# Optimization experiments

Measured on AMD Instinct MI355X. Metric: run time of the kernel, lower is better.

## Reference

```python
import jax, jax.numpy as jnp
import numpy as np

HEADS = 8

def setup_inputs() -> dict:
    key = jax.random.key(0)
    ks = jax.random.split(key, 6)
    N, C, L = 8, 512, 2048
    s = 0.02
    return {
        'x':  jax.random.normal(ks[0], (N, C, L), dtype=jnp.float32),
        'Wq': jax.random.normal(ks[1], (C, C), dtype=jnp.float32) * s,
        'Wk': jax.random.normal(ks[2], (C, C), dtype=jnp.float32) * s,
        'Wv': jax.random.normal(ks[3], (C, C), dtype=jnp.float32) * s,
        'Wo': jax.random.normal(ks[4], (C, C), dtype=jnp.float32) * s,
        'bo': jnp.zeros((C,), dtype=jnp.float32),
    }

def reference(x, Wq, Wk, Wv, Wo, bo):
    N, C, L = x.shape
    h = HEADS
    d = C // h
    scale = C ** (-0.5)  # note: scales by full channels, as in the original

    def proj(W):
        # Conv1d(k=1, bias=False) == per-position linear: [N,C,L] -> [N,L,h,d]
        y = jnp.einsum('oc,ncl->nlo', W, x)
        return y.reshape(N, L, h, d)

    q, k, v = proj(Wq), proj(Wk), proj(Wv)

    qk = jnp.einsum('nqhd,nkhd->nhqk', q, k)  # [N,h,L,L]
    causal_mask = jnp.tril(jnp.ones((L, L), dtype=bool))
    qk = jnp.where(causal_mask, qk, -jnp.inf)
    attn = jax.nn.softmax(qk * scale, axis=-1)

    out = jnp.einsum('nhqk,nkhd->nqhd', attn, v)  # [N,L,h,d]
    out = out.reshape(N, L, C).transpose(0, 2, 1)  # n (h d) l
    return jnp.einsum('oc,ncl->nol', Wo, out) + bo[None, :, None]
```

## Files before the change

### kernel.cpp

```cpp
#include <hip/hip_runtime.h>
#include <math.h>

typedef __bf16 bf16;
typedef __attribute__((ext_vector_type(8))) __bf16 bf16x8;
typedef __attribute__((ext_vector_type(4))) float f32x4;
typedef unsigned short u16;
typedef unsigned int u32;

constexpr int Nn = 8, Cc = 512, Ll = 2048, Hh = 8, Dd = 64;
constexpr float kScale = 0.044194173824159216f;
constexpr float kQexp2 = kScale * 1.44269504088896341f;
constexpr size_t NCL = (size_t)Nn * Cc * Ll;
constexpr size_t WSZ = (size_t)Cc * Cc;

static __device__ __forceinline__ u16 bfbits(bf16 v) {
    union { bf16 b; u16 u; } x; x.b = v; return x.u;
}
static __device__ __forceinline__ u32 fbits(float f) {
    union { float f; u32 u; } x; x.f = f; return x.u;
}
static __device__ __forceinline__ float fexp2(float x) {
#if __has_builtin(__builtin_amdgcn_exp2f)
    return __builtin_amdgcn_exp2f(x);
#else
    return exp2f(x);
#endif
}

#define MFMA(a, b, c) __builtin_amdgcn_mfma_f32_16x16x32_bf16((a), (b), (c), 0, 0, 0)

static __device__ __forceinline__ void async16(const bf16* g, bf16* l) {
    __builtin_amdgcn_global_load_lds(
        (const __attribute__((address_space(1))) void*)g,
        (__attribute__((address_space(3))) void*)l, 16, 0, 0);
}

__global__ __launch_bounds__(256) void xpose_kernel(
    const float* __restrict__ x, bf16* __restrict__ xT)
{
    __shared__ bf16 Ts[64][72];
    const int lt = blockIdx.x, ct = blockIdx.y, n = blockIdx.z;
    const int tid = threadIdx.x;

    const int cr = tid >> 2, l0 = (tid & 3) * 16;
    const float* src = x + ((size_t)(n * Cc + ct * 64 + cr)) * Ll + lt * 64 + l0;
#pragma unroll
    for (int i = 0; i < 4; i++) {
        float4 v = *(const float4*)(src + i * 4);
        Ts[l0 + i * 4 + 0][cr] = (bf16)v.x;
        Ts[l0 + i * 4 + 1][cr] = (bf16)v.y;
        Ts[l0 + i * 4 + 2][cr] = (bf16)v.z;
        Ts[l0 + i * 4 + 3][cr] = (bf16)v.w;
    }
    __syncthreads();

    const int lr = tid >> 2, c0 = (tid & 3) * 16;
    bf16* dst = xT + ((size_t)(n * Ll + lt * 64 + lr)) * Cc + ct * 64 + c0;
    *(bf16x8*)(dst)     = *(const bf16x8*)&Ts[lr][c0];
    *(bf16x8*)(dst + 8) = *(const bf16x8*)&Ts[lr][c0 + 8];
}

__global__ __launch_bounds__(256) void cvtw_kernel(
    const float* __restrict__ Wq, const float* __restrict__ Wk,
    const float* __restrict__ Wv, const float* __restrict__ Wo,
    bf16* __restrict__ Wb)
{
    size_t i = (size_t)blockIdx.x * 256 + threadIdx.x;
    int w = (int)(i >> 16);
    size_t o = i & 65535;
    const float* src = (w == 0) ? Wq : (w == 1) ? Wk : (w == 2) ? Wv : Wo;
    float4 v = ((const float4*)src)[o];
    ushort4 u;
    u.x = bfbits((bf16)v.x); u.y = bfbits((bf16)v.y);
    u.z = bfbits((bf16)v.z); u.w = bfbits((bf16)v.w);
    *(ushort4*)(Wb + (size_t)w * WSZ + o * 4) = u;
}

__global__ __launch_bounds__(256) void qkv_gemm(
    const bf16* __restrict__ xT, const bf16* __restrict__ Wb,
    bf16* __restrict__ Qt, bf16* __restrict__ Kt, bf16* __restrict__ Vb)
{
    const int lt = blockIdx.x, ow = blockIdx.y, n = blockIdx.z;
    const int widx = ow >> 2, otile = ow & 3;

    __shared__ bf16 Xs[128 * 64];
    __shared__ bf16 Ws[128 * 64];

    const int tid = threadIdx.x;
    const int lane = tid & 63, wv = tid >> 6;
    const int m = lane & 15, quad = lane >> 4;
    const int rh = wv & 1, ch = wv >> 1;

    const bf16* __restrict__ W = Wb + (size_t)widx * WSZ + (size_t)otile * 128 * Cc;
    const bf16* __restrict__ X = xT + (size_t)(n * Ll + lt * 128) * Cc;

    int srow[4], scol[4];
#pragma unroll
    for (int i = 0; i < 4; i++) {
        int q = i * 256 + tid;
        srow[i] = q >> 3;
        scol[i] = ((q ^ (q >> 3)) & 7) * 8;
    }

    f32x4 acc[4][4] = {};

    for (int c0 = 0; c0 < Cc; c0 += 64) {
#pragma unroll
        for (int i = 0; i < 4; i++)
            async16(&X[(size_t)srow[i] * Cc + c0 + scol[i]], &Xs[(i * 256 + tid) * 8]);
#pragma unroll
        for (int i = 0; i < 4; i++)
            async16(&W[(size_t)srow[i] * Cc + c0 + scol[i]], &Ws[(i * 256 + tid) * 8]);
        __syncthreads();

        const bf16* TA = (widx < 2) ? Xs : Ws;
        const bf16* TB = (widx < 2) ? Ws : Xs;
#pragma unroll
        for (int kk = 0; kk < 2; kk++) {
            const int sw = (((kk * 4 + quad) ^ (m & 7)) * 8);
            bf16x8 af[4], bfr[4];
#pragma unroll
            for (int t = 0; t < 4; t++)
                af[t] = *(const bf16x8*)&TA[(rh * 64 + t * 16 + m) * 64 + sw];
#pragma unroll
            for (int u = 0; u < 4; u++)
                bfr[u] = *(const bf16x8*)&TB[(ch * 64 + u * 16 + m) * 64 + sw];
#pragma unroll
            for (int t = 0; t < 4; t++)
#pragma unroll
                for (int u = 0; u < 4; u++)
                    acc[t][u] = MFMA(af[t], bfr[u], acc[t][u]);
        }
        __syncthreads();
    }

    if (widx < 2) {
        const float fq = (widx == 0) ? kQexp2 : 1.0f;
        bf16* __restrict__ OUT = (widx == 0) ? Qt : Kt;
#pragma unroll
        for (int u = 0; u < 4; u++) {
            const int o = otile * 128 + ch * 64 + u * 16 + m;
            const int h = o >> 6, d = o & 63;
            bf16* base = OUT + (size_t)(n * Hh + h) * Ll * Dd + d;
#pragma unroll
            for (int t = 0; t < 4; t++) {
                const int l0 = lt * 128 + rh * 64 + t * 16 + quad * 4;
#pragma unroll
                for (int r = 0; r < 4; r++)
                    base[(size_t)(l0 + r) * Dd] = (bf16)(acc[t][u][r] * fq);
            }
        }
    } else {
#pragma unroll
        for (int t = 0; t < 4; t++) {
            const int ob = otile * 128 + rh * 64 + t * 16 + quad * 4;
#pragma unroll
            for (int r = 0; r < 4; r++) {
                const int oo = ob + r, h = oo >> 6, d = oo & 63;
                bf16* base = Vb + ((size_t)(n * Hh + h) * Dd + d) * Ll;
#pragma unroll
                for (int u = 0; u < 4; u++)
                    base[lt * 128 + ch * 64 + u * 16 + m] = (bf16)acc[t][u][r];
            }
        }
    }
}

__global__ __launch_bounds__(512, 4) void attn_mfma(
    const bf16* __restrict__ Qt, const bf16* __restrict__ Kt,
    const bf16* __restrict__ Vb, bf16* __restrict__ AO)
{
    const int h  = blockIdx.x;
    const int jp = blockIdx.y;
    const int n  = blockIdx.z;

    __shared__ bf16 KV[2][2][64 * 72];
    __shared__ bf16 Pbuf[8][16 * 72];

    const int tid = threadIdx.x;
    const int lane = tid & 63, wv = tid >> 6;
    const int m = lane & 15, quad = lane >> 4;

    const size_t bnh = (size_t)(n * Hh + h) * Ll * Dd;
    const bf16* __restrict__ Qh = Qt + bnh;
    const bf16* __restrict__ Kh = Kt + bnh;
    const bf16* __restrict__ Vh = Vb + bnh;

    const int srow = tid >> 3;
    const int sc8  = (tid & 7) * 8;

    bf16* const Pw = &Pbuf[wv][0];

    bf16x8 ones;
#pragma unroll
    for (int j = 0; j < 8; j++) ones[j] = (bf16)1.0f;

    int koff[4];
#pragma unroll
    for (int r = 0; r < 4; r++) koff[r] = quad * 4 + r - m;

#pragma unroll 1
    for (int ph = 0; ph < 2; ph++) {
        const int st = ph ? (15 - jp) : jp;
        const int R  = st * 128;
        const int nk = 2 * st + 2;
        const int qrow0 = R + wv * 16;

        bf16x8 qf0 = *(const bf16x8*)&Qh[(size_t)(qrow0 + m) * Dd + quad * 8];
        bf16x8 qf1 = *(const bf16x8*)&Qh[(size_t)(qrow0 + m) * Dd + 32 + quad * 8];

        f32x4 O[4] = {};
        f32x4 Ls = {};

        {
            bf16x8 ka = *(const bf16x8*)&Kh[(size_t)srow * Dd + sc8];
            bf16x8 va = *(const bf16x8*)&Vh[(size_t)srow * Ll + sc8];
            *(bf16x8*)&KV[0][0][srow * 72 + sc8] = ka;
            *(bf16x8*)&KV[0][1][srow * 72 + sc8] = va;
        }
        __syncthreads();

        for (int kt = 0; kt < nk; kt++) {
            const int cur = kt & 1, nxt = cur ^ 1;
            const int kb = kt * 64;
            const bool do_pf = (kt + 1 < nk);

            bf16x8 ka, va;
            if (do_pf) {
                const int kn = kb + 64;
                ka = *(const bf16x8*)&Kh[(size_t)(kn + srow) * Dd + sc8];
                va = *(const bf16x8*)&Vh[(size_t)srow * Ll + kn + sc8];
            }

            const bool skip = (kb > qrow0 + 15);
            if (!skip) {
                const bf16* Ks = &KV[cur][0][0];
                const bf16* Vs = &KV[cur][1][0];

                f32x4 St[4] = {};
#pragma unroll
                for (int t = 0; t < 4; t++) {
                    bf16x8 kf0 = *(const bf16x8*)&Ks[(t * 16 + m) * 72 + quad * 8];
                    bf16x8 kf1 = *(const bf16x8*)&Ks[(t * 16 + m) * 72 + 32 + quad * 8];
                    St[t] = MFMA(kf0, qf0, St[t]);
                    St[t] = MFMA(kf1, qf1, St[t]);
                }

                const bool dg = (kb + 63 > qrow0);
                const int thr = qrow0 - kb;
#pragma unroll
                for (int t = 0; t < 4; t++) {
                    float p0 = fexp2(St[t][0]);
                    float p1 = fexp2(St[t][1]);
                    float p2 = fexp2(St[t][2]);
                    float p3 = fexp2(St[t][3]);
                    if (dg) {
                        if (t * 16 + koff[0] > thr) p0 = 0.f;
                        if (t * 16 + koff[1] > thr) p1 = 0.f;
                        if (t * 16 + koff[2] > thr) p2 = 0.f;
                        if (t * 16 + koff[3] > thr) p3 = 0.f;
                    }
                    u32 pk0 = (fbits(p0) >> 16) | (fbits(p1) & 0xFFFF0000u);
                    u32 pk1 = (fbits(p2) >> 16) | (fbits(p3) & 0xFFFF0000u);
                    *(uint2*)&Pw[m * 72 + t * 16 + quad * 4] = make_uint2(pk0, pk1);
                }
                asm volatile("s_waitcnt lgkmcnt(0)" ::: "memory");

                bf16x8 pf0 = *(const bf16x8*)&Pw[m * 72 + quad * 8];
                bf16x8 pf1 = *(const bf16x8*)&Pw[m * 72 + 32 + quad * 8];

                Ls = MFMA(pf0, ones, Ls);
                Ls = MFMA(pf1, ones, Ls);
#pragma unroll
                for (int t = 0; t < 4; t++) {
                    bf16x8 vf0 = *(const bf16x8*)&Vs[(t * 16 + m) * 72 + quad * 8];
                    bf16x8 vf1 = *(const bf16x8*)&Vs[(t * 16 + m) * 72 + 32 + quad * 8];
                    O[t] = MFMA(pf0, vf0, O[t]);
                    O[t] = MFMA(pf1, vf1, O[t]);
                }
            }

            __syncthreads();
            if (do_pf) {
                *(bf16x8*)&KV[nxt][0][srow * 72 + sc8] = ka;
                *(bf16x8*)&KV[nxt][1][srow * 72 + sc8] = va;
                __syncthreads();
            }
        }

        f32x4 inv;
#pragma unroll
        for (int r = 0; r < 4; r++) inv[r] = 1.0f / Ls[r];

        const size_t aobase = (size_t)n * Ll * Cc + (size_t)h * 64;
#pragma unroll
        for (int t = 0; t < 4; t++)
#pragma unroll
            for (int r = 0; r < 4; r++) {
                const int q = qrow0 + quad * 4 + r;
                AO[aobase + (size_t)q * Cc + t * 16 + m] = (bf16)(O[t][r] * inv[r]);
            }
        __syncthreads();
    }
}

__global__ __launch_bounds__(256) void out_gemm(
    const bf16* __restrict__ AO, const bf16* __restrict__ Wb,
    const float* __restrict__ bo, float* __restrict__ out)
{
    const int lt = blockIdx.x, ot = blockIdx.y, n = blockIdx.z;

    __shared__ bf16 Ws[128 * 64];
    __shared__ bf16 Bs[128 * 64];

    const int tid = threadIdx.x;
    const int lane = tid & 63, wv = tid >> 6;
    const int m = lane & 15, quad = lane >> 4;
    const int rh = wv & 1, ch = wv >> 1;

    const bf16* __restrict__ W = Wb + 3 * WSZ + (size_t)ot * 128 * Cc;
    const bf16* __restrict__ B = AO + (size_t)(n * Ll + lt * 128) * Cc;

    int srow[4], scol[4];
#pragma unroll
    for (int i = 0; i < 4; i++) {
        int q = i * 256 + tid;
        srow[i] = q >> 3;
        scol[i] = ((q ^ (q >> 3)) & 7) * 8;
    }

    f32x4 acc[4][4] = {};

    for (int c0 = 0; c0 < Cc; c0 += 64) {
#pragma unroll
        for (int i = 0; i < 4; i++)
            async16(&W[(size_t)srow[i] * Cc + c0 + scol[i]], &Ws[(i * 256 + tid) * 8]);
#pragma unroll
        for (int i = 0; i < 4; i++)
            async16(&B[(size_t)srow[i] * Cc + c0 + scol[i]], &Bs[(i * 256 + tid) * 8]);
        __syncthreads();

#pragma unroll
        for (int kk = 0; kk < 2; kk++) {
            const int sw = (((kk * 4 + quad) ^ (m & 7)) * 8);
            bf16x8 af[4], bfr[4];
#pragma unroll
            for (int t = 0; t < 4; t++)
                af[t] = *(const bf16x8*)&Ws[(rh * 64 + t * 16 + m) * 64 + sw];
#pragma unroll
            for (int u = 0; u < 4; u++)
                bfr[u] = *(const bf16x8*)&Bs[(ch * 64 + u * 16 + m) * 64 + sw];
#pragma unroll
            for (int t = 0; t < 4; t++)
#pragma unroll
                for (int u = 0; u < 4; u++)
                    acc[t][u] = MFMA(af[t], bfr[u], acc[t][u]);
        }
        __syncthreads();
    }

#pragma unroll
    for (int t = 0; t < 4; t++) {
        const int ob = ot * 128 + rh * 64 + t * 16 + quad * 4;
#pragma unroll
        for (int r = 0; r < 4; r++) {
            const int o = ob + r;
            const float b = bo[o];
            float* base = out + ((size_t)n * Cc + o) * Ll + lt * 128 + ch * 64;
#pragma unroll
            for (int u = 0; u < 4; u++)
                base[u * 16 + m] = acc[t][u][r] + b;
        }
    }
}

extern "C" void kernel_launch(void* const* d_in, const int* in_sizes, int n_in,
                              void* d_out, int out_size, void* d_ws, size_t ws_size,
                              hipStream_t stream)
{
    const float* x  = (const float*)d_in[0];
    const float* Wq = (const float*)d_in[1];
    const float* Wk = (const float*)d_in[2];
    const float* Wv = (const float*)d_in[3];
    const float* Wo = (const float*)d_in[4];
    const float* bo = (const float*)d_in[5];
    float* out = (float*)d_out;

    bf16* ws = (bf16*)d_ws;
    bf16* xT = ws;
    bf16* Wb = xT + NCL;
    bf16* Qt = Wb + 4 * WSZ;
    bf16* Kt = Qt + NCL;
    bf16* Vb = Kt + NCL;
    bf16* AO = Vb + NCL;

    xpose_kernel<<<dim3(32, 8, Nn), 256, 0, stream>>>(x, xT);
    cvtw_kernel<<<1024, 256, 0, stream>>>(Wq, Wk, Wv, Wo, Wb);
    qkv_gemm<<<dim3(16, 12, Nn), 256, 0, stream>>>(xT, Wb, Qt, Kt, Vb);
    attn_mfma<<<dim3(Hh, 8, Nn), 512, 0, stream>>>(Qt, Kt, Vb, AO);
    out_gemm<<<dim3(16, 4, Nn), 256, 0, stream>>>(AO, Wb, bo, out);
}
```

Baseline: 204.2 us.

## Async global-to-LDS K/V loads with XOR swizzle, smaller attention tiles, fuse prep kernels

The attention kernel now uses 256-thread blocks over 64-row query tiles with 32 tile pairs, which removes the fully masked key-tile iterations the 128-row tiles carried. K/V tiles go straight from global memory into an unpadded, XOR-swizzled LDS buffer through global_load_lds, replacing the register-staged copy and its second barrier per iteration. The weight conversion is folded into the transpose kernel as an extra grid slice, saving one launch. The trade-off is more blocks and per-block Q loads, and correctness depends on the async loads finishing before the next barrier.

```diff
diff --git a/kernel.cpp b/kernel.cpp
--- a/kernel.cpp
+++ b/kernel.cpp
@@ -35,12 +35,32 @@
         (__attribute__((address_space(3))) void*)l, 16, 0, 0);
 }
 
-__global__ __launch_bounds__(256) void xpose_kernel(
-    const float* __restrict__ x, bf16* __restrict__ xT)
-{
+__global__ __launch_bounds__(256) void prep_kernel(
+    const float* __restrict__ x,
+    const float* __restrict__ Wq, const float* __restrict__ Wk,
+    const float* __restrict__ Wv, const float* __restrict__ Wo,
+    bf16* __restrict__ xT, bf16* __restrict__ Wb)
+{
+    const int tid = threadIdx.x;
+    if (blockIdx.z == Nn) {
+        int gid = (blockIdx.y * 32 + blockIdx.x) * 256 + tid;
+        int w = gid >> 14;
+        int o = (gid & 16383) * 4;
+        const float* src = (w == 0) ? Wq : (w == 1) ? Wk : (w == 2) ? Wv : Wo;
+        bf16* dst = Wb + (size_t)w * WSZ;
+#pragma unroll
+        for (int j = 0; j < 4; j++) {
+            float4 v = ((const float4*)src)[o + j];
+            ushort4 u;
+            u.x = bfbits((bf16)v.x); u.y = bfbits((bf16)v.y);
+            u.z = bfbits((bf16)v.z); u.w = bfbits((bf16)v.w);
+            *(ushort4*)(dst + (size_t)(o + j) * 4) = u;
+        }
+        return;
+    }
+
     __shared__ bf16 Ts[64][72];
     const int lt = blockIdx.x, ct = blockIdx.y, n = blockIdx.z;
-    const int tid = threadIdx.x;
 
     const int cr = tid >> 2, l0 = (tid & 3) * 16;
     const float* src = x + ((size_t)(n * Cc + ct * 64 + cr)) * Ll + lt * 64 + l0;
@@ -60,22 +80,6 @@
     *(bf16x8*)(dst + 8) = *(const bf16x8*)&Ts[lr][c0 + 8];
 }
 
-__global__ __launch_bounds__(256) void cvtw_kernel(
-    const float* __restrict__ Wq, const float* __restrict__ Wk,
-    const float* __restrict__ Wv, const float* __restrict__ Wo,
-    bf16* __restrict__ Wb)
-{
-    size_t i = (size_t)blockIdx.x * 256 + threadIdx.x;
-    int w = (int)(i >> 16);
-    size_t o = i & 65535;
-    const float* src = (w == 0) ? Wq : (w == 1) ? Wk : (w == 2) ? Wv : Wo;
-    float4 v = ((const float4*)src)[o];
-    ushort4 u;
-    u.x = bfbits((bf16)v.x); u.y = bfbits((bf16)v.y);
-    u.z = bfbits((bf16)v.z); u.w = bfbits((bf16)v.w);
-    *(ushort4*)(Wb + (size_t)w * WSZ + o * 4) = u;
-}
-
 __global__ __launch_bounds__(256) void qkv_gemm(
     const bf16* __restrict__ xT, const bf16* __restrict__ Wb,
     bf16* __restrict__ Qt, bf16* __restrict__ Kt, bf16* __restrict__ Vb)
@@ -166,7 +170,7 @@
     }
 }
 
-__global__ __launch_bounds__(512, 4) void attn_mfma(
+__global__ __launch_bounds__(256, 4) void attn_mfma(
     const bf16* __restrict__ Qt, const bf16* __restrict__ Kt,
     const bf16* __restrict__ Vb, bf16* __restrict__ AO)
 {
@@ -174,8 +178,8 @@
     const int jp = blockIdx.y;
     const int n  = blockIdx.z;
 
-    __shared__ bf16 KV[2][2][64 * 72];
-    __shared__ bf16 Pbuf[8][16 * 72];
+    __shared__ bf16 KV[2][2][64 * 64];
+    __shared__ bf16 Pbuf[4][16 * 64];
 
     const int tid = threadIdx.x;
     const int lane = tid & 63, wv = tid >> 6;
@@ -187,7 +191,8 @@
     const bf16* __restrict__ Vh = Vb + bnh;
 
     const int srow = tid >> 3;
-    const int sc8  = (tid & 7) * 8;
+    const int scs  = (((tid & 7) ^ (srow & 7)) * 8);
+    const int swz  = (m & 7);
 
     bf16* const Pw = &Pbuf[wv][0];
 
@@ -195,16 +200,16 @@
 #pragma unroll
     for (int j = 0; j < 8; j++) ones[j] = (bf16)1.0f;
 
+    const int thr = 16 * wv;
     int koff[4];
 #pragma unroll
     for (int r = 0; r < 4; r++) koff[r] = quad * 4 + r - m;
 
 #pragma unroll 1
     for (int ph = 0; ph < 2; ph++) {
-        const int st = ph ? (15 - jp) : jp;
-        const int R  = st * 128;
-        const int nk = 2 * st + 2;
-        const int qrow0 = R + wv * 16;
+        const int st = ph ? (31 - jp) : jp;
+        const int nk = st + 1;
+        const int qrow0 = st * 64 + wv * 16;
 
         bf16x8 qf0 = *(const bf16x8*)&Qh[(size_t)(qrow0 + m) * Dd + quad * 8];
         bf16x8 qf1 = *(const bf16x8*)&Qh[(size_t)(qrow0 + m) * Dd + 32 + quad * 8];
@@ -212,80 +217,69 @@
         f32x4 O[4] = {};
         f32x4 Ls = {};
 
-        {
-            bf16x8 ka = *(const bf16x8*)&Kh[(size_t)srow * Dd + sc8];
-            bf16x8 va = *(const bf16x8*)&Vh[(size_t)srow * Ll + sc8];
-            *(bf16x8*)&KV[0][0][srow * 72 + sc8] = ka;
-            *(bf16x8*)&KV[0][1][srow * 72 + sc8] = va;
-        }
+        async16(&Kh[(size_t)(srow) * Dd + scs],      &KV[0][0][(size_t)tid * 8]);
+        async16(&Kh[(size_t)(srow + 32) * Dd + scs], &KV[0][0][(size_t)tid * 8 + 2048]);
+        async16(&Vh[(size_t)srow * Ll + scs],        &KV[0][1][(size_t)tid * 8]);
+        async16(&Vh[(size_t)(srow + 32) * Ll + scs], &KV[0][1][(size_t)tid * 8 + 2048]);
         __syncthreads();
 
         for (int kt = 0; kt < nk; kt++) {
-            const int cur = kt & 1, nxt = cur ^ 1;
-            const int kb = kt * 64;
-            const bool do_pf = (kt + 1 < nk);
-
-            bf16x8 ka, va;
-            if (do_pf) {
-                const int kn = kb + 64;
-                ka = *(const bf16x8*)&Kh[(size_t)(kn + srow) * Dd + sc8];
-                va = *(const bf16x8*)&Vh[(size_t)srow * Ll + kn + sc8];
-            }
-
-            const bool skip = (kb > qrow0 + 15);
-            if (!skip) {
-                const bf16* Ks = &KV[cur][0][0];
-                const bf16* Vs = &KV[cur][1][0];
-
-                f32x4 St[4] = {};
-#pragma unroll
-                for (int t = 0; t < 4; t++) {
-                    bf16x8 kf0 = *(const bf16x8*)&Ks[(t * 16 + m) * 72 + quad * 8];
-                    bf16x8 kf1 = *(const bf16x8*)&Ks[(t * 16 + m) * 72 + 32 + quad * 8];
-                    St[t] = MFMA(kf0, qf0, St[t]);
-                    St[t] = MFMA(kf1, qf1, St[t]);
+            const int cur = kt & 1;
+
+            if (kt + 1 < nk) {
+                const int kn = (kt + 1) * 64;
+                async16(&Kh[(size_t)(kn + srow) * Dd + scs],      &KV[cur ^ 1][0][(size_t)tid * 8]);
+                async16(&Kh[(size_t)(kn + srow + 32) * Dd + scs], &KV[cur ^ 1][0][(size_t)tid * 8 + 2048]);
+                async16(&Vh[(size_t)srow * Ll + kn + scs],        &KV[cur ^ 1][1][(size_t)tid * 8]);
+                async16(&Vh[(size_t)(srow + 32) * Ll + kn + scs], &KV[cur ^ 1][1][(size_t)tid * 8 + 2048]);
+            }
+
+            const bf16* Ks = &KV[cur][0][0];
+            const bf16* Vs = &KV[cur][1][0];
+
+            f32x4 St[4] = {};
+#pragma unroll
+            for (int t = 0; t < 4; t++) {
+                bf16x8 kf0 = *(const bf16x8*)&Ks[(t * 16 + m) * 64 + ((quad ^ swz) * 8)];
+                bf16x8 kf1 = *(const bf16x8*)&Ks[(t * 16 + m) * 64 + (((4 + quad) ^ swz) * 8)];
+                St[t] = MFMA(kf0, qf0, St[t]);
+                St[t] = MFMA(kf1, qf1, St[t]);
+            }
+
+            const bool dg = (kt == st);
+#pragma unroll
+            for (int t = 0; t < 4; t++) {
+                float p0 = fexp2(St[t][0]);
+                float p1 = fexp2(St[t][1]);
+                float p2 = fexp2(St[t][2]);
+                float p3 = fexp2(St[t][3]);
+                if (dg) {
+                    if (t * 16 + koff[0] > thr) p0 = 0.f;
+                    if (t * 16 + koff[1] > thr) p1 = 0.f;
+                    if (t * 16 + koff[2] > thr) p2 = 0.f;
+                    if (t * 16 + koff[3] > thr) p3 = 0.f;
                 }
-
-                const bool dg = (kb + 63 > qrow0);
-                const int thr = qrow0 - kb;
-#pragma unroll
-                for (int t = 0; t < 4; t++) {
-                    float p0 = fexp2(St[t][0]);
-                    float p1 = fexp2(St[t][1]);
-                    float p2 = fexp2(St[t][2]);
-                    float p3 = fexp2(St[t][3]);
-                    if (dg) {
-                        if (t * 16 + koff[0] > thr) p0 = 0.f;
-                        if (t * 16 + koff[1] > thr) p1 = 0.f;
-                        if (t * 16 + koff[2] > thr) p2 = 0.f;
-                        if (t * 16 + koff[3] > thr) p3 = 0.f;
-                    }
-                    u32 pk0 = (fbits(p0) >> 16) | (fbits(p1) & 0xFFFF0000u);
-                    u32 pk1 = (fbits(p2) >> 16) | (fbits(p3) & 0xFFFF0000u);
-                    *(uint2*)&Pw[m * 72 + t * 16 + quad * 4] = make_uint2(pk0, pk1);
-                }
-                asm volatile("s_waitcnt lgkmcnt(0)" ::: "memory");
-
-                bf16x8 pf0 = *(const bf16x8*)&Pw[m * 72 + quad * 8];
-                bf16x8 pf1 = *(const bf16x8*)&Pw[m * 72 + 32 + quad * 8];
-
-                Ls = MFMA(pf0, ones, Ls);
-                Ls = MFMA(pf1, ones, Ls);
-#pragma unroll
-                for (int t = 0; t < 4; t++) {
-                    bf16x8 vf0 = *(const bf16x8*)&Vs[(t * 16 + m) * 72 + quad * 8];
-                    bf16x8 vf1 = *(const bf16x8*)&Vs[(t * 16 + m) * 72 + 32 + quad * 8];
-                    O[t] = MFMA(pf0, vf0, O[t]);
-                    O[t] = MFMA(pf1, vf1, O[t]);
-                }
+                u32 pk0 = (fbits(p0) >> 16) | (fbits(p1) & 0xFFFF0000u);
+                u32 pk1 = (fbits(p2) >> 16) | (fbits(p3) & 0xFFFF0000u);
+                const int pidx = m * 64 + (((2 * t + (quad >> 1)) ^ swz) * 8) + (quad & 1) * 4;
+                *(uint2*)&Pw[pidx] = make_uint2(pk0, pk1);
+            }
+            asm volatile("s_waitcnt lgkmcnt(0)" ::: "memory");
+
+            bf16x8 pf0 = *(const bf16x8*)&Pw[m * 64 + ((quad ^ swz) * 8)];
+            bf16x8 pf1 = *(const bf16x8*)&Pw[m * 64 + (((4 + quad) ^ swz) * 8)];
+
+            Ls = MFMA(pf0, ones, Ls);
+            Ls = MFMA(pf1, ones, Ls);
+#pragma unroll
+            for (int t = 0; t < 4; t++) {
+                bf16x8 vf0 = *(const bf16x8*)&Vs[(t * 16 + m) * 64 + ((quad ^ swz) * 8)];
+                bf16x8 vf1 = *(const bf16x8*)&Vs[(t * 16 + m) * 64 + (((4 + quad) ^ swz) * 8)];
+                O[t] = MFMA(pf0, vf0, O[t]);
+                O[t] = MFMA(pf1, vf1, O[t]);
             }
 
             __syncthreads();
-            if (do_pf) {
-                *(bf16x8*)&KV[nxt][0][srow * 72 + sc8] = ka;
-                *(bf16x8*)&KV[nxt][1][srow * 72 + sc8] = va;
-                __syncthreads();
-            }
         }
 
         f32x4 inv;
@@ -300,7 +294,6 @@
                 const int q = qrow0 + quad * 4 + r;
                 AO[aobase + (size_t)q * Cc + t * 16 + m] = (bf16)(O[t][r] * inv[r]);
             }
-        __syncthreads();
     }
 }
 
@@ -394,9 +387,8 @@
     bf16* Vb = Kt + NCL;
     bf16* AO = Vb + NCL;
 
-    xpose_kernel<<<dim3(32, 8, Nn), 256, 0, stream>>>(x, xT);
-    cvtw_kernel<<<1024, 256, 0, stream>>>(Wq, Wk, Wv, Wo, Wb);
+    prep_kernel<<<dim3(32, 8, Nn + 1), 256, 0, stream>>>(x, Wq, Wk, Wv, Wo, xT, Wb);
     qkv_gemm<<<dim3(16, 12, Nn), 256, 0, stream>>>(xT, Wb, Qt, Kt, Vb);
-    attn_mfma<<<dim3(Hh, 8, Nn), 512, 0, stream>>>(Qt, Kt, Vb, AO);
+    attn_mfma<<<dim3(Hh, 16, Nn), 256, 0, stream>>>(Qt, Kt, Vb, AO);
     out_gemm<<<dim3(16, 4, Nn), 256, 0, stream>>>(AO, Wb, bo, out);
 }
```

Result: faster. 195.5 us (-4.3%).
